# Performance work log

Measured on AMD Instinct MI355X. Metric: run time of the kernel, lower is better.

Reference implementation:

```python
import jax, jax.numpy as jnp
import numpy as np

B, T, DIM = 2, 4096, 2048
H, HKV = 16, 4
HD = DIM // H          # 128
NREP = H // HKV        # 4
R = 16                 # csa_compress_ratio
TOPK = 64              # min(csa_top_k, max_seq_len // R)
THETA = 10000.0


def setup_inputs() -> dict:
    key = jax.random.key(0)
    ks = jax.random.split(key, 9)
    s = 0.02
    return {
        "x":   jax.random.normal(ks[0], (B, T, DIM), jnp.float32),
        "wq":  jax.random.normal(ks[1], (DIM, H * HD),  jnp.float32) * s,
        "wk":  jax.random.normal(ks[2], (DIM, HKV * HD), jnp.float32) * s,
        "wv":  jax.random.normal(ks[3], (DIM, HKV * HD), jnp.float32) * s,
        "wo":  jax.random.normal(ks[4], (DIM, DIM), jnp.float32) * s,
        "wiq": jax.random.normal(ks[5], (DIM, HD), jnp.float32) * s,
        "wik": jax.random.normal(ks[6], (DIM, HD), jnp.float32) * s,
        "cwa": jax.random.normal(ks[7], (HD,), jnp.float32) * s,
        "cwb": jax.random.normal(ks[8], (HD,), jnp.float32) * s,
    }


def _rope(x, cos, sin):
    # x: [B, h, T, HD]; pairs (x[2i], x[2i+1]) rotated by angle[t, i]
    half = HD // 2
    xr = x.reshape(*x.shape[:-1], half, 2)
    a, b = xr[..., 0], xr[..., 1]          # [B, h, T, half]
    ra = a * cos - b * sin                 # cos/sin: [T, half] broadcast
    rb = a * sin + b * cos
    return jnp.stack([ra, rb], axis=-1).reshape(x.shape)


def reference(x, wq, wk, wv, wo, wiq, wik, cwa, cwb):
    Bx, Tx, C = x.shape
    half = HD // 2
    # RoPE tables (buffer in original, deterministic -> recomputed here)
    freqs = 1.0 / (THETA ** (jnp.arange(half, dtype=jnp.float32) / half))
    ang = jnp.arange(Tx, dtype=jnp.float32)[:, None] * freqs[None, :]  # [T, half]
    cos, sin = jnp.cos(ang), jnp.sin(ang)

    q = (x @ wq).reshape(Bx, Tx, H, HD).transpose(0, 2, 1, 3)    # [B,H,T,HD]
    k = (x @ wk).reshape(Bx, Tx, HKV, HD).transpose(0, 2, 1, 3)  # [B,HKV,T,HD]
    v = (x @ wv).reshape(Bx, Tx, HKV, HD).transpose(0, 2, 1, 3)
    q = _rope(q, cos, sin)
    k = _rope(k, cos, sin)

    # chunked softmax-weighted KV compression (vectorized over blocks)
    nb = Tx // R
    kb = k.reshape(Bx, HKV, nb, R, HD)
    vb = v.reshape(Bx, HKV, nb, R, HD)
    wa = jax.nn.softmax(kb @ cwa, axis=-1)   # [B,HKV,nb,R], softmax within block
    wb_ = jax.nn.softmax(kb @ cwb, axis=-1)
    w = 0.5 * (wa + wb_)
    ck = jnp.einsum('bhnr,bhnrd->bhnd', w, kb)  # [B,HKV,nb,HD]
    cv = jnp.einsum('bhnr,bhnrd->bhnd', w, vb)

    # indexer: scores[b,t] = mean_j( qi[b,t] . ki[b,j] ) = qi[b,t] . mean_j ki[b,j]
    qi = x @ wiq                         # [B,T,HD]
    ki_mean = (x @ wik).mean(axis=1)     # [B,HD]
    scores = jnp.einsum('btd,bd->bt', qi, ki_mean)  # [B,T]
    block_scores = scores[:, :nb]                   # [B,nb]

    if nb > TOPK:
        idx = jax.lax.top_k(block_scores, TOPK)[1]             # [B,TOPK]
        ck = jnp.take_along_axis(ck, idx[:, None, :, None], axis=2)  # [B,HKV,TOPK,HD]
        cv = jnp.take_along_axis(cv, idx[:, None, :, None], axis=2)

    # GQA repeat + sparse attention over selected compressed blocks (no mask)
    k_rep = jnp.repeat(ck, NREP, axis=1)   # [B,H,TOPK,HD]
    v_rep = jnp.repeat(cv, NREP, axis=1)
    att = jax.nn.softmax(
        jnp.einsum('bhtd,bhsd->bhts', q, k_rep) / jnp.sqrt(jnp.float32(HD)),
        axis=-1)                            # [B,H,T,TOPK]
    out = jnp.einsum('bhts,bhsd->bhtd', att, v_rep)
    out = out.transpose(0, 2, 1, 3).reshape(Bx, Tx, C)
    return out @ wo
```

## Files before the change

### kernel.cpp

```cpp
#include <hip/hip_runtime.h>
#include <math.h>
#include <stdint.h>

#define BB    2
#define TT    4096
#define CDIM  2048
#define NHQ   16
#define NKV   4
#define HD    128
#define HALF  64
#define NREP  4
#define RBLK  16
#define NB    256
#define TOPK  64

#define MROWS (BB * TT)
#define NQKV  (CDIM + 2 * NKV * HD)
#define XELE  ((size_t)MROWS * CDIM)

typedef __bf16 bf16;
typedef __bf16 bf16x4 __attribute__((ext_vector_type(4)));
typedef __bf16 bf16x8 __attribute__((ext_vector_type(8)));
typedef float f32x4 __attribute__((ext_vector_type(4)));

typedef __attribute__((address_space(1))) unsigned int gu32;
typedef __attribute__((address_space(3))) unsigned int lu32;

__device__ __forceinline__ void gload_lds16(const void* g, void* l) {
  void* gv = const_cast<void*>(g);
  __builtin_amdgcn_global_load_lds((gu32*)gv, (lu32*)l, 16, 0, 0);
}

__device__ __forceinline__ void mfma3_core(const bf16* __restrict__ Ah,
                                           const bf16* __restrict__ Al,
                                           const bf16* __restrict__ Bh,
                                           const bf16* __restrict__ Bl,
                                           int K, int bm, int bn,
                                           f32x4 acc[8][4]) {
  __shared__ bf16 sAh[256 * 32];
  __shared__ bf16 sAl[256 * 32];
  __shared__ bf16 sBh[128 * 32];
  __shared__ bf16 sBl[128 * 32];
  const int tid = threadIdx.x;
  const int wave = tid >> 6, lane = tid & 63;
  const int wr = wave >> 1, wc = wave & 1;
  const int fr = lane & 15, lg = lane >> 4;
  const int lr4 = lane >> 2;
  const int cgs = (lane & 3) ^ ((lane >> 3) & 3);
  const size_t stageoff = (size_t)lr4 * K + cgs * 8;

  const bf16* gAh = Ah + (size_t)bm * K + stageoff;
  const bf16* gAl = Al + (size_t)bm * K + stageoff;
  const bf16* gBh = Bh + (size_t)bn * K + stageoff;
  const bf16* gBl = Bl + (size_t)bn * K + stageoff;

  const int swf = (fr >> 1) & 3;
  const int aoffe = (wr * 128 + fr) * 32 + ((lg ^ swf) << 3);
  const int boffe = (wc * 64 + fr) * 32 + ((lg ^ swf) << 3);

  for (int k0 = 0; k0 < K; k0 += 32) {
    __syncthreads();
    if (wave == 0) {
#pragma unroll
      for (int u = 0; u < 12; ++u)
        gload_lds16(gAh + (size_t)(u * 16) * K + k0, sAh + u * 512);
    } else if (wave == 1) {
#pragma unroll
      for (int u = 12; u < 16; ++u)
        gload_lds16(gAh + (size_t)(u * 16) * K + k0, sAh + u * 512);
#pragma unroll
      for (int u = 0; u < 8; ++u)
        gload_lds16(gAl + (size_t)(u * 16) * K + k0, sAl + u * 512);
    } else if (wave == 2) {
#pragma unroll
      for (int u = 8; u < 16; ++u)
        gload_lds16(gAl + (size_t)(u * 16) * K + k0, sAl + u * 512);
#pragma unroll
      for (int u = 0; u < 4; ++u)
        gload_lds16(gBh + (size_t)(u * 16) * K + k0, sBh + u * 512);
    } else {
#pragma unroll
      for (int u = 4; u < 8; ++u)
        gload_lds16(gBh + (size_t)(u * 16) * K + k0, sBh + u * 512);
#pragma unroll
      for (int u = 0; u < 8; ++u)
        gload_lds16(gBl + (size_t)(u * 16) * K + k0, sBl + u * 512);
    }
    __syncthreads();
    bf16x8 fah[8], fal[8];
#pragma unroll
    for (int i = 0; i < 8; ++i) {
      fah[i] = *(const bf16x8*)&sAh[aoffe + i * 512];
      fal[i] = *(const bf16x8*)&sAl[aoffe + i * 512];
    }
#pragma unroll
    for (int j = 0; j < 4; ++j) {
      bf16x8 fbh = *(const bf16x8*)&sBh[boffe + j * 512];
      bf16x8 fbl = *(const bf16x8*)&sBl[boffe + j * 512];
#pragma unroll
      for (int i = 0; i < 8; ++i) {
        acc[i][j] = __builtin_amdgcn_mfma_f32_16x16x32_bf16(fah[i], fbh, acc[i][j], 0, 0, 0);
        acc[i][j] = __builtin_amdgcn_mfma_f32_16x16x32_bf16(fah[i], fbl, acc[i][j], 0, 0, 0);
        acc[i][j] = __builtin_amdgcn_mfma_f32_16x16x32_bf16(fal[i], fbh, acc[i][j], 0, 0, 0);
      }
    }
  }
}

__global__ __launch_bounds__(256, 2) void csa_gemm_qkv(const bf16* __restrict__ xh,
                                                       const bf16* __restrict__ xl,
                                                       const bf16* __restrict__ wth,
                                                       const bf16* __restrict__ wtl,
                                                       float* __restrict__ qb,
                                                       float* __restrict__ kb,
                                                       float* __restrict__ vb) {
  f32x4 acc[8][4] = {};
  const int bm = blockIdx.y << 8, bn = blockIdx.x << 7;
  mfma3_core(xh, xl, wth, wtl, CDIM, bm, bn, acc);
  const int wave = threadIdx.x >> 6, lane = threadIdx.x & 63;
  const int wr = wave >> 1, wc = wave & 1;
  const int fr = lane & 15, lg = lane >> 4;
  float* dst; int ncols, colofs;
  if (bn < CDIM)            { dst = qb; ncols = CDIM; colofs = bn; }
  else if (bn < CDIM + 512) { dst = kb; ncols = 512;  colofs = bn - CDIM; }
  else                      { dst = vb; ncols = 512;  colofs = bn - CDIM - 512; }
#pragma unroll
  for (int i = 0; i < 8; ++i)
#pragma unroll
    for (int j = 0; j < 4; ++j) {
      int row0 = bm + wr * 128 + i * 16 + (lg << 2);
      int col = colofs + wc * 64 + j * 16 + fr;
#pragma unroll
      for (int r = 0; r < 4; ++r)
        dst[(size_t)(row0 + r) * ncols + col] = acc[i][j][r];
    }
}

__global__ __launch_bounds__(256, 2) void csa_gemm_wo(const bf16* __restrict__ ah,
                                                      const bf16* __restrict__ al,
                                                      const bf16* __restrict__ wth,
                                                      const bf16* __restrict__ wtl,
                                                      float* __restrict__ C) {
  f32x4 acc[8][4] = {};
  const int bm = blockIdx.y << 8, bn = blockIdx.x << 7;
  mfma3_core(ah, al, wth, wtl, CDIM, bm, bn, acc);
  const int wave = threadIdx.x >> 6, lane = threadIdx.x & 63;
  const int wr = wave >> 1, wc = wave & 1;
  const int fr = lane & 15, lg = lane >> 4;
#pragma unroll
  for (int i = 0; i < 8; ++i)
#pragma unroll
    for (int j = 0; j < 4; ++j) {
      int row0 = bm + wr * 128 + i * 16 + (lg << 2);
      int col = bn + wc * 64 + j * 16 + fr;
#pragma unroll
      for (int r = 0; r < 4; ++r)
        C[(size_t)(row0 + r) * CDIM + col] = acc[i][j][r];
    }
}

__global__ void csa_xconv(const float4* __restrict__ x, bf16x4* __restrict__ xh,
                          bf16x4* __restrict__ xl) {
  int i = blockIdx.x * 256 + threadIdx.x;
  float4 v = x[i];
  bf16x4 h, l;
  h[0] = (bf16)v.x; l[0] = (bf16)(v.x - (float)h[0]);
  h[1] = (bf16)v.y; l[1] = (bf16)(v.y - (float)h[1]);
  h[2] = (bf16)v.z; l[2] = (bf16)(v.z - (float)h[2]);
  h[3] = (bf16)v.w; l[3] = (bf16)(v.w - (float)h[3]);
  xh[i] = h;
  xl[i] = l;
}

__global__ __launch_bounds__(256) void csa_wconv(const float* __restrict__ W, int N,
                                                 bf16* __restrict__ wth,
                                                 bf16* __restrict__ wtl, int rowofs) {
  __shared__ float tile[32][33];
  int k0 = blockIdx.y * 32, n0 = blockIdx.x * 32;
  int tx = threadIdx.x & 31, ty = threadIdx.x >> 5;
#pragma unroll
  for (int r = 0; r < 32; r += 8)
    tile[ty + r][tx] = W[(size_t)(k0 + ty + r) * N + n0 + tx];
  __syncthreads();
#pragma unroll
  for (int r = 0; r < 32; r += 8) {
    int n = ty + r;
    float x = tile[tx][n];
    bf16 h = (bf16)x;
    bf16 l = (bf16)(x - (float)h);
    size_t o = (size_t)(rowofs + n0 + n) * CDIM + k0 + tx;
    wth[o] = h;
    wtl[o] = l;
  }
}

__global__ void csa_rope_table(float* __restrict__ cost, float* __restrict__ sint) {
  int idx = blockIdx.x * blockDim.x + threadIdx.x;
  if (idx >= TT * HALF) return;
  int t = idx / HALF, i = idx % HALF;
  double freq = pow(10000.0, -(double)i / (double)HALF);
  double ang = (double)t * freq;
  cost[idx] = (float)cos(ang);
  sint[idx] = (float)sin(ang);
}

__global__ void csa_rope_apply(float* __restrict__ buf, const float* __restrict__ cost,
                               const float* __restrict__ sint, int nheads, int total) {
  int idx = blockIdx.x * blockDim.x + threadIdx.x;
  if (idx >= total) return;
  int i = idx % HALF;
  int h = (idx / HALF) % nheads;
  int t = (idx / (HALF * nheads)) % TT;
  int b = idx / (HALF * nheads * TT);
  float c = cost[t * HALF + i], s = sint[t * HALF + i];
  float* p = buf + ((((size_t)b * TT + t) * nheads + h) * HD) + 2 * i;
  float a = p[0], q = p[1];
  p[0] = a * c - q * s;
  p[1] = a * s + q * c;
}

__global__ void csa_xpart(const float* __restrict__ x, float* __restrict__ xpart) {
  int d = blockIdx.x * 256 + threadIdx.x;
  int ts = blockIdx.y;
  int b = blockIdx.z;
  float s = 0.f;
  int t0 = ts * (TT / 16);
  for (int t = t0; t < t0 + TT / 16; ++t) s += x[((size_t)b * TT + t) * CDIM + d];
  xpart[((size_t)b * 16 + ts) * CDIM + d] = s;
}

__global__ void csa_kimean(const float* __restrict__ xpart, const float* __restrict__ wik,
                           float* __restrict__ ki) {
  int b = blockIdx.x >> 7;
  int j = blockIdx.x & 127;
  int tid = threadIdx.x;
  float s = 0.f;
  for (int d = tid; d < CDIM; d += 256) {
    float xm = 0.f;
#pragma unroll
    for (int ts = 0; ts < 16; ++ts) xm += xpart[((size_t)b * 16 + ts) * CDIM + d];
    s += xm * wik[(size_t)d * HD + j];
  }
  __shared__ float red[256];
  red[tid] = s;
  __syncthreads();
  for (int off = 128; off > 0; off >>= 1) {
    if (tid < off) red[tid] += red[tid + off];
    __syncthreads();
  }
  if (tid == 0) ki[b * HD + j] = red[0] * (1.f / (float)TT);
}

__global__ void csa_u(const float* __restrict__ wiq, const float* __restrict__ ki,
                      float* __restrict__ u) {
  int idx = blockIdx.x * 256 + threadIdx.x;
  int b = idx / CDIM, d = idx % CDIM;
  float s = 0.f;
#pragma unroll 8
  for (int j = 0; j < HD; ++j) s += wiq[(size_t)d * HD + j] * ki[b * HD + j];
  u[idx] = s;
}

__global__ void csa_scores(const float* __restrict__ x, const float* __restrict__ u,
                           float* __restrict__ sc) {
  int b = blockIdx.x >> 8;
  int t = blockIdx.x & 255;
  int tid = threadIdx.x;
  float s = 0.f;
  for (int d = tid; d < CDIM; d += 256)
    s += x[((size_t)b * TT + t) * CDIM + d] * u[b * CDIM + d];
  __shared__ float red[256];
  red[tid] = s;
  __syncthreads();
  for (int off = 128; off > 0; off >>= 1) {
    if (tid < off) red[tid] += red[tid + off];
    __syncthreads();
  }
  if (tid == 0) sc[blockIdx.x] = red[0];
}

__global__ void csa_topk(const float* __restrict__ sc, int* __restrict__ topk) {
  __shared__ float val[NB];
  __shared__ float rv[256];
  __shared__ int ri[256];
  int b = blockIdx.x, tid = threadIdx.x;
  val[tid] = sc[b * NB + tid];
  __syncthreads();
  for (int it = 0; it < TOPK; ++it) {
    rv[tid] = val[tid];
    ri[tid] = tid;
    __syncthreads();
    for (int off = 128; off > 0; off >>= 1) {
      if (tid < off) {
        if (rv[tid + off] > rv[tid] ||
            (rv[tid + off] == rv[tid] && ri[tid + off] < ri[tid])) {
          rv[tid] = rv[tid + off];
          ri[tid] = ri[tid + off];
        }
      }
      __syncthreads();
    }
    if (tid == 0) {
      topk[b * TOPK + it] = ri[0];
      val[ri[0]] = -INFINITY;
    }
    __syncthreads();
  }
}

__global__ __launch_bounds__(64) void csa_compress(const float* __restrict__ kbuf,
                                                   const float* __restrict__ vbuf,
                                                   const int* __restrict__ topk,
                                                   const float* __restrict__ cwa,
                                                   const float* __restrict__ cwb,
                                                   bf16* __restrict__ ckh,
                                                   bf16* __restrict__ ckl,
                                                   bf16* __restrict__ cvth,
                                                   bf16* __restrict__ cvtl) {
  int blk = blockIdx.x;
  int b = blk / (NKV * TOPK);
  int h = (blk / TOPK) % NKV;
  int j = blk % TOPK;
  int n = topk[b * TOPK + j];
  int l = threadIdx.x;
  float ca0 = cwa[l], ca1 = cwa[l + 64];
  float cb0 = cwb[l], cb1 = cwb[l + 64];
  float kk[RBLK][2], vv[RBLK][2], ar[RBLK], br[RBLK];
#pragma unroll
  for (int r = 0; r < RBLK; ++r) {
    int t = n * RBLK + r;
    size_t base = (((size_t)b * TT + t) * NKV + h) * HD;
    kk[r][0] = kbuf[base + l];
    kk[r][1] = kbuf[base + l + 64];
    vv[r][0] = vbuf[base + l];
    vv[r][1] = vbuf[base + l + 64];
    float pa = kk[r][0] * ca0 + kk[r][1] * ca1;
    float pb = kk[r][0] * cb0 + kk[r][1] * cb1;
    for (int off = 32; off > 0; off >>= 1) {
      pa += __shfl_xor(pa, off);
      pb += __shfl_xor(pb, off);
    }
    ar[r] = pa;
    br[r] = pb;
  }
  float ma = -INFINITY, mb = -INFINITY;
#pragma unroll
  for (int r = 0; r < RBLK; ++r) { ma = fmaxf(ma, ar[r]); mb = fmaxf(mb, br[r]); }
  float ea[RBLK], eb[RBLK], sa = 0.f, sb = 0.f;
#pragma unroll
  for (int r = 0; r < RBLK; ++r) {
    ea[r] = expf(ar[r] - ma); sa += ea[r];
    eb[r] = expf(br[r] - mb); sb += eb[r];
  }
  float isa = 1.f / sa, isb = 1.f / sb;
  float o0 = 0.f, o1 = 0.f, p0 = 0.f, p1 = 0.f;
#pragma unroll
  for (int r = 0; r < RBLK; ++r) {
    float w = 0.5f * (ea[r] * isa + eb[r] * isb);
    o0 += w * kk[r][0]; o1 += w * kk[r][1];
    p0 += w * vv[r][0]; p1 += w * vv[r][1];
  }
  size_t ckbase = ((size_t)(b * NKV + h) * 64 + j) * 128;
  bf16 h0 = (bf16)o0; ckh[ckbase + l] = h0;      ckl[ckbase + l] = (bf16)(o0 - (float)h0);
  bf16 h1 = (bf16)o1; ckh[ckbase + l + 64] = h1; ckl[ckbase + l + 64] = (bf16)(o1 - (float)h1);
  size_t vtbase = (size_t)(b * NKV + h) * (128 * 64);
  bf16 g0 = (bf16)p0; cvth[vtbase + (size_t)l * 64 + j] = g0;
  cvtl[vtbase + (size_t)l * 64 + j] = (bf16)(p0 - (float)g0);
  bf16 g1 = (bf16)p1; cvth[vtbase + (size_t)(l + 64) * 64 + j] = g1;
  cvtl[vtbase + (size_t)(l + 64) * 64 + j] = (bf16)(p1 - (float)g1);
}

__global__ __launch_bounds__(256) void csa_attn_mfma(const float* __restrict__ qb,
                                                     const float* __restrict__ cost,
                                                     const float* __restrict__ sint,
                                                     const bf16* __restrict__ ckh_g,
                                                     const bf16* __restrict__ ckl_g,
                                                     const bf16* __restrict__ cvth_g,
                                                     const bf16* __restrict__ cvtl_g,
                                                     bf16* __restrict__ oh_g,
                                                     bf16* __restrict__ ol_g) {
  __shared__ __align__(16) bf16 sck[2][64 * 128];
  __shared__ __align__(16) bf16 sV[2][64 * 64];
  const int tid = threadIdx.x;
  const int wave = tid >> 6, lane = tid & 63;
  const int b = blockIdx.y >> 2, kvh = blockIdx.y & 3;
  const int row0 = blockIdx.x << 7;
  const int wrow = wave << 5;
  const int lr = lane & 15, lg = lane >> 4;
  const float scale = 0.08838834764831845f;

  const bf16* gkh = ckh_g + (size_t)(b * NKV + kvh) * (64 * 128);
  const bf16* gkl = ckl_g + (size_t)(b * NKV + kvh) * (64 * 128);
  const bf16* gvh = cvth_g + (size_t)(b * NKV + kvh) * (128 * 64);
  const bf16* gvl = cvtl_g + (size_t)(b * NKV + kvh) * (128 * 64);

  for (int idx = tid; idx < 1024; idx += 256) {
    int j = idx >> 4, c = idx & 15;
    int dst = (j * 16 + (c ^ (j & 15))) * 8;
    *(uint4*)&sck[0][dst] = *(const uint4*)(gkh + j * 128 + c * 8);
    *(uint4*)&sck[1][dst] = *(const uint4*)(gkl + j * 128 + c * 8);
  }
  for (int idx = tid; idx < 512; idx += 256) {
    int d = idx >> 3, c = idx & 7;
    int dst = (d * 8 + (c ^ (d & 7))) * 8;
    *(uint4*)&sV[0][dst] = *(const uint4*)(gvh + d * 64 + c * 8);
    *(uint4*)&sV[1][dst] = *(const uint4*)(gvl + d * 64 + c * 8);
  }

  bf16x8 qfh[2][4], qfl[2][4];
#pragma unroll
  for (int it = 0; it < 2; ++it)
#pragma unroll
    for (int ks = 0; ks < 4; ++ks) {
      int row = wrow + it * 16 + lr;
      int g = row0 + row;
      int t = g >> 2;
      int hh = kvh * NREP + (g & 3);
      int d0 = ks * 32 + (lg << 3);
      const float* qp = qb + (((size_t)b * TT + t) * NHQ + hh) * HD + d0;
      float4 a = *(const float4*)qp;
      float4 b4 = *(const float4*)(qp + 4);
      float4 cs = *(const float4*)&cost[t * HALF + (d0 >> 1)];
      float4 sn = *(const float4*)&sint[t * HALF + (d0 >> 1)];
      float f[8];
      f[0] = a.x * cs.x - a.y * sn.x;  f[1] = a.x * sn.x + a.y * cs.x;
      f[2] = a.z * cs.y - a.w * sn.y;  f[3] = a.z * sn.y + a.w * cs.y;
      f[4] = b4.x * cs.z - b4.y * sn.z; f[5] = b4.x * sn.z + b4.y * cs.z;
      f[6] = b4.z * cs.w - b4.w * sn.w; f[7] = b4.z * sn.w + b4.w * cs.w;
      bf16x8 h8, l8;
#pragma unroll
      for (int u = 0; u < 8; ++u) {
        h8[u] = (bf16)f[u];
        l8[u] = (bf16)(f[u] - (float)h8[u]);
      }
      qfh[it][ks] = h8;
      qfl[it][ks] = l8;
    }
  __syncthreads();

  f32x4 accS[2][4] = {};
#pragma unroll
  for (int ks = 0; ks < 4; ++ks) {
    bf16x8 kh[4], kl[4];
#pragma unroll
    for (int jt = 0; jt < 4; ++jt) {
      int row = jt * 16 + lr;
      int c = ks * 4 + lg;
      int off = (row * 16 + (c ^ (row & 15))) * 8;
      kh[jt] = *(const bf16x8*)&sck[0][off];
      kl[jt] = *(const bf16x8*)&sck[1][off];
    }
#pragma unroll
    for (int it = 0; it < 2; ++it)
#pragma unroll
      for (int jt = 0; jt < 4; ++jt) {
        accS[it][jt] = __builtin_amdgcn_mfma_f32_16x16x32_bf16(qfh[it][ks], kh[jt], accS[it][jt], 0, 0, 0);
        accS[it][jt] = __builtin_amdgcn_mfma_f32_16x16x32_bf16(qfh[it][ks], kl[jt], accS[it][jt], 0, 0, 0);
        accS[it][jt] = __builtin_amdgcn_mfma_f32_16x16x32_bf16(qfl[it][ks], kh[jt], accS[it][jt], 0, 0, 0);
      }
  }

#pragma unroll
  for (int it = 0; it < 2; ++it)
#pragma unroll
    for (int r = 0; r < 4; ++r) {
      float v0 = accS[it][0][r] * scale, v1 = accS[it][1][r] * scale;
      float v2 = accS[it][2][r] * scale, v3 = accS[it][3][r] * scale;
      float m = fmaxf(fmaxf(v0, v1), fmaxf(v2, v3));
      for (int off = 8; off > 0; off >>= 1) m = fmaxf(m, __shfl_xor(m, off));
      float e0 = expf(v0 - m), e1 = expf(v1 - m), e2 = expf(v2 - m), e3 = expf(v3 - m);
      float s = e0 + e1 + e2 + e3;
      for (int off = 8; off > 0; off >>= 1) s += __shfl_xor(s, off);
      float inv = 1.f / s;
      accS[it][0][r] = e0 * inv; accS[it][1][r] = e1 * inv;
      accS[it][2][r] = e2 * inv; accS[it][3][r] = e3 * inv;
    }

  __syncthreads();

#pragma unroll
  for (int it = 0; it < 2; ++it)
#pragma unroll
    for (int jt = 0; jt < 4; ++jt)
#pragma unroll
      for (int r = 0; r < 4; ++r) {
        int row = wrow + it * 16 + (lg << 2) + r;
        int k = jt * 16 + lr;
        float p = accS[it][jt][r];
        bf16 ph = (bf16)p;
        int c = k >> 3;
        int off = (row * 8 + (c ^ (row & 7))) * 8 + (k & 7);
        sck[0][off] = ph;
        sck[1][off] = (bf16)(p - (float)ph);
      }
  __syncthreads();

  for (int half = 0; half < 2; ++half) {
    if (half) {
      __syncthreads();
      for (int idx = tid; idx < 512; idx += 256) {
        int d = idx >> 3, c = idx & 7;
        int dst = (d * 8 + (c ^ (d & 7))) * 8;
        *(uint4*)&sV[0][dst] = *(const uint4*)(gvh + (64 + d) * 64 + c * 8);
        *(uint4*)&sV[1][dst] = *(const uint4*)(gvl + (64 + d) * 64 + c * 8);
      }
      __syncthreads();
    }
    f32x4 accO[2][4] = {};
#pragma unroll
    for (int ks = 0; ks < 2; ++ks) {
      bf16x8 pah[2], pal[2], vh[4], vl[4];
#pragma unroll
      for (int it = 0; it < 2; ++it) {
        int row = wrow + it * 16 + lr;
        int c = ks * 4 + lg;
        int off = (row * 8 + (c ^ (row & 7))) * 8;
        pah[it] = *(const bf16x8*)&sck[0][off];
        pal[it] = *(const bf16x8*)&sck[1][off];
      }
#pragma unroll
      for (int jt = 0; jt < 4; ++jt) {
        int d = jt * 16 + lr;
        int c = ks * 4 + lg;
        int off = (d * 8 + (c ^ (d & 7))) * 8;
        vh[jt] = *(const bf16x8*)&sV[0][off];
        vl[jt] = *(const bf16x8*)&sV[1][off];
      }
#pragma unroll
      for (int it = 0; it < 2; ++it)
#pragma unroll
        for (int jt = 0; jt < 4; ++jt) {
          accO[it][jt] = __builtin_amdgcn_mfma_f32_16x16x32_bf16(pah[it], vh[jt], accO[it][jt], 0, 0, 0);
          accO[it][jt] = __builtin_amdgcn_mfma_f32_16x16x32_bf16(pah[it], vl[jt], accO[it][jt], 0, 0, 0);
          accO[it][jt] = __builtin_amdgcn_mfma_f32_16x16x32_bf16(pal[it], vh[jt], accO[it][jt], 0, 0, 0);
        }
    }
#pragma unroll
    for (int it = 0; it < 2; ++it)
#pragma unroll
      for (int jt = 0; jt < 4; ++jt)
#pragma unroll
        for (int r = 0; r < 4; ++r) {
          int row = wrow + it * 16 + (lg << 2) + r;
          int g = row0 + row;
          int t = g >> 2;
          int hh = kvh * NREP + (g & 3);
          size_t ob = (((size_t)b * TT + t) * NHQ + hh) * HD + half * 64 + jt * 16 + lr;
          float o = accO[it][jt][r];
          bf16 oh = (bf16)o;
          oh_g[ob] = oh;
          ol_g[ob] = (bf16)(o - (float)oh);
        }
  }
}

extern "C" void kernel_launch(void* const* d_in, const int* in_sizes, int n_in,
                              void* d_out, int out_size, void* d_ws, size_t ws_size,
                              hipStream_t stream) {
  const float* x   = (const float*)d_in[0];
  const float* wq  = (const float*)d_in[1];
  const float* wk  = (const float*)d_in[2];
  const float* wv  = (const float*)d_in[3];
  const float* wo  = (const float*)d_in[4];
  const float* wiq = (const float*)d_in[5];
  const float* wik = (const float*)d_in[6];
  const float* cwa = (const float*)d_in[7];
  const float* cwb = (const float*)d_in[8];
  float* out = (float*)d_out;

  float* qb = out;

  float* ws = (float*)d_ws;
  float* kb   = ws;
  float* vb   = kb + (size_t)MROWS * 512;
  bf16*  xh   = (bf16*)(vb + (size_t)MROWS * 512);
  bf16*  xl   = xh + XELE;
  bf16*  wqh  = xl + XELE;
  bf16*  wql  = wqh + (size_t)NQKV * CDIM;
  float* cost = (float*)(wql + (size_t)NQKV * CDIM);
  float* sint = cost + (size_t)TT * HALF;
  float* xpart = sint + (size_t)TT * HALF;
  float* ki   = xpart + (size_t)BB * 16 * CDIM;
  float* u    = ki + BB * HD;
  float* sc   = u + BB * CDIM;
  bf16*  ckh  = (bf16*)(sc + BB * NB);
  bf16*  ckl  = ckh + (size_t)BB * NKV * 64 * 128;
  bf16*  cvth = ckl + (size_t)BB * NKV * 64 * 128;
  bf16*  cvtl = cvth + (size_t)BB * NKV * 128 * 64;
  int* topk   = (int*)(cvtl + (size_t)BB * NKV * 128 * 64);
  bf16* oh  = xh;
  bf16* ol_ = xl;
  bf16* woh = wqh;
  bf16* wol = wql;

  csa_xconv<<<(XELE / 4) / 256, 256, 0, stream>>>((const float4*)x, (bf16x4*)xh, (bf16x4*)xl);
  csa_wconv<<<dim3(CDIM / 32, CDIM / 32), 256, 0, stream>>>(wq, CDIM, wqh, wql, 0);
  csa_wconv<<<dim3(512 / 32, CDIM / 32), 256, 0, stream>>>(wk, 512, wqh, wql, CDIM);
  csa_wconv<<<dim3(512 / 32, CDIM / 32), 256, 0, stream>>>(wv, 512, wqh, wql, CDIM + 512);

  csa_gemm_qkv<<<dim3(NQKV / 128, MROWS / 256), 256, 0, stream>>>(xh, xl, wqh, wql, qb, kb, vb);

  csa_wconv<<<dim3(CDIM / 32, CDIM / 32), 256, 0, stream>>>(wo, CDIM, woh, wol, 0);

  csa_rope_table<<<(TT * HALF + 255) / 256, 256, 0, stream>>>(cost, sint);
  csa_rope_apply<<<(BB * TT * NKV * HALF + 255) / 256, 256, 0, stream>>>(kb, cost, sint, NKV, BB * TT * NKV * HALF);

  csa_xpart<<<dim3(CDIM / 256, 16, BB), 256, 0, stream>>>(x, xpart);
  csa_kimean<<<BB * HD, 256, 0, stream>>>(xpart, wik, ki);
  csa_u<<<(BB * CDIM) / 256, 256, 0, stream>>>(wiq, ki, u);
  csa_scores<<<BB * NB, 256, 0, stream>>>(x, u, sc);
  csa_topk<<<BB, 256, 0, stream>>>(sc, topk);

  csa_compress<<<BB * NKV * TOPK, 64, 0, stream>>>(kb, vb, topk, cwa, cwb, ckh, ckl, cvth, cvtl);

  csa_attn_mfma<<<dim3((TT * NREP) / 128, BB * NKV), 256, 0, stream>>>(qb, cost, sint, ckh, ckl, cvth, cvtl, oh, ol_);

  csa_gemm_wo<<<dim3(CDIM / 128, MROWS / 256), 256, 0, stream>>>(oh, ol_, woh, wol, out);
}
```

Before: 792.1 us.

## Double-buffer GEMM LDS tiles with 8-wave blocks and async prefetch

```diff
diff --git a/kernel.cpp b/kernel.cpp
--- a/kernel.cpp
+++ b/kernel.cpp
@@ -31,92 +31,104 @@
   __builtin_amdgcn_global_load_lds((gu32*)gv, (lu32*)l, 16, 0, 0);
 }
 
-__device__ __forceinline__ void mfma3_core(const bf16* __restrict__ Ah,
-                                           const bf16* __restrict__ Al,
-                                           const bf16* __restrict__ Bh,
-                                           const bf16* __restrict__ Bl,
-                                           int K, int bm, int bn,
-                                           f32x4 acc[8][4]) {
-  __shared__ bf16 sAh[256 * 32];
-  __shared__ bf16 sAl[256 * 32];
-  __shared__ bf16 sBh[128 * 32];
-  __shared__ bf16 sBl[128 * 32];
+
+#define LDS_BUF 24576
+#define OFF_AL  8192
+#define OFF_BH  16384
+#define OFF_BL  20480
+
+__device__ __forceinline__ void mfma3_step(const bf16* __restrict__ sb, int arow,
+                                           int brow, int chunk, f32x4 acc[4][4]) {
+  bf16x8 fah[4], fal[4], fbh[4], fbl[4];
+#pragma unroll
+  for (int i = 0; i < 4; ++i) {
+    fah[i] = *(const bf16x8*)&sb[(arow + i * 16) * 32 + chunk];
+    fal[i] = *(const bf16x8*)&sb[OFF_AL + (arow + i * 16) * 32 + chunk];
+  }
+#pragma unroll
+  for (int j = 0; j < 4; ++j) {
+    fbh[j] = *(const bf16x8*)&sb[OFF_BH + (brow + j * 16) * 32 + chunk];
+    fbl[j] = *(const bf16x8*)&sb[OFF_BL + (brow + j * 16) * 32 + chunk];
+  }
+  __builtin_amdgcn_s_setprio(1);
+#pragma unroll
+  for (int j = 0; j < 4; ++j)
+#pragma unroll
+    for (int i = 0; i < 4; ++i) {
+      acc[i][j] = __builtin_amdgcn_mfma_f32_16x16x32_bf16(fah[i], fbh[j], acc[i][j], 0, 0, 0);
+      acc[i][j] = __builtin_amdgcn_mfma_f32_16x16x32_bf16(fah[i], fbl[j], acc[i][j], 0, 0, 0);
+      acc[i][j] = __builtin_amdgcn_mfma_f32_16x16x32_bf16(fal[i], fbh[j], acc[i][j], 0, 0, 0);
+    }
+  __builtin_amdgcn_s_setprio(0);
+}
+
+__device__ __forceinline__ void mfma3_core8(const bf16* __restrict__ Ah,
+                                            const bf16* __restrict__ Al,
+                                            const bf16* __restrict__ Bh,
+                                            const bf16* __restrict__ Bl,
+                                            int bm, int bn,
+                                            f32x4 acc[4][4]) {
+  __shared__ __align__(16) bf16 smem[2 * LDS_BUF];
   const int tid = threadIdx.x;
   const int wave = tid >> 6, lane = tid & 63;
+  const int lr4 = lane >> 2;
+  const int cgs = (lane & 3) ^ ((lane >> 3) & 3);
+  const size_t stageoff = (size_t)lr4 * CDIM + cgs * 8;
+
+  const bf16* gp[6];
+  int loff[6];
+#pragma unroll
+  for (int u = 0; u < 6; ++u) {
+    int c = wave * 6 + u;
+    const bf16* base;
+    int lbase;
+    if (c < 16)      { base = Ah + (size_t)(bm + c * 16) * CDIM;        lbase = c * 512; }
+    else if (c < 32) { base = Al + (size_t)(bm + (c - 16) * 16) * CDIM; lbase = OFF_AL + (c - 16) * 512; }
+    else if (c < 40) { base = Bh + (size_t)(bn + (c - 32) * 16) * CDIM; lbase = OFF_BH + (c - 32) * 512; }
+    else             { base = Bl + (size_t)(bn + (c - 40) * 16) * CDIM; lbase = OFF_BL + (c - 40) * 512; }
+    gp[u] = base + stageoff;
+    loff[u] = lbase;
+  }
+
   const int wr = wave >> 1, wc = wave & 1;
   const int fr = lane & 15, lg = lane >> 4;
-  const int lr4 = lane >> 2;
-  const int cgs = (lane & 3) ^ ((lane >> 3) & 3);
-  const size_t stageoff = (size_t)lr4 * K + cgs * 8;
-
-  const bf16* gAh = Ah + (size_t)bm * K + stageoff;
-  const bf16* gAl = Al + (size_t)bm * K + stageoff;
-  const bf16* gBh = Bh + (size_t)bn * K + stageoff;
-  const bf16* gBl = Bl + (size_t)bn * K + stageoff;
-
-  const int swf = (fr >> 1) & 3;
-  const int aoffe = (wr * 128 + fr) * 32 + ((lg ^ swf) << 3);
-  const int boffe = (wc * 64 + fr) * 32 + ((lg ^ swf) << 3);
-
-  for (int k0 = 0; k0 < K; k0 += 32) {
-    __syncthreads();
-    if (wave == 0) {
-#pragma unroll
-      for (int u = 0; u < 12; ++u)
-        gload_lds16(gAh + (size_t)(u * 16) * K + k0, sAh + u * 512);
-    } else if (wave == 1) {
-#pragma unroll
-      for (int u = 12; u < 16; ++u)
-        gload_lds16(gAh + (size_t)(u * 16) * K + k0, sAh + u * 512);
-#pragma unroll
-      for (int u = 0; u < 8; ++u)
-        gload_lds16(gAl + (size_t)(u * 16) * K + k0, sAl + u * 512);
-    } else if (wave == 2) {
-#pragma unroll
-      for (int u = 8; u < 16; ++u)
-        gload_lds16(gAl + (size_t)(u * 16) * K + k0, sAl + u * 512);
-#pragma unroll
-      for (int u = 0; u < 4; ++u)
-        gload_lds16(gBh + (size_t)(u * 16) * K + k0, sBh + u * 512);
-    } else {
-#pragma unroll
-      for (int u = 4; u < 8; ++u)
-        gload_lds16(gBh + (size_t)(u * 16) * K + k0, sBh + u * 512);
-#pragma unroll
-      for (int u = 0; u < 8; ++u)
-        gload_lds16(gBl + (size_t)(u * 16) * K + k0, sBl + u * 512);
-    }
-    __syncthreads();
-    bf16x8 fah[8], fal[8];
-#pragma unroll
-    for (int i = 0; i < 8; ++i) {
-      fah[i] = *(const bf16x8*)&sAh[aoffe + i * 512];
-      fal[i] = *(const bf16x8*)&sAl[aoffe + i * 512];
-    }
-#pragma unroll
-    for (int j = 0; j < 4; ++j) {
-      bf16x8 fbh = *(const bf16x8*)&sBh[boffe + j * 512];
-      bf16x8 fbl = *(const bf16x8*)&sBl[boffe + j * 512];
-#pragma unroll
-      for (int i = 0; i < 8; ++i) {
-        acc[i][j] = __builtin_amdgcn_mfma_f32_16x16x32_bf16(fah[i], fbh, acc[i][j], 0, 0, 0);
-        acc[i][j] = __builtin_amdgcn_mfma_f32_16x16x32_bf16(fah[i], fbl, acc[i][j], 0, 0, 0);
-        acc[i][j] = __builtin_amdgcn_mfma_f32_16x16x32_bf16(fal[i], fbh, acc[i][j], 0, 0, 0);
-      }
-    }
-  }
-}
-
-__global__ __launch_bounds__(256, 2) void csa_gemm_qkv(const bf16* __restrict__ xh,
+  const int chunk = (lg ^ ((fr >> 1) & 3)) << 3;
+  const int arow = wr * 64 + fr;
+  const int brow = wc * 64 + fr;
+
+#pragma unroll
+  for (int u = 0; u < 6; ++u) gload_lds16(gp[u], &smem[loff[u]]);
+
+  for (int t = 0; t < 63; ++t) {
+    const int nbase = ((t + 1) & 1) * LDS_BUF;
+    const int kk = (t + 1) * 32;
+#pragma unroll
+    for (int u = 0; u < 6; ++u) gload_lds16(gp[u] + kk, &smem[nbase + loff[u]]);
+    asm volatile("s_waitcnt vmcnt(6)" ::: "memory");
+    __builtin_amdgcn_s_barrier();
+    asm volatile("" ::: "memory");
+
+    mfma3_step(&smem[(t & 1) * LDS_BUF], arow, brow, chunk, acc);
+
+    asm volatile("" ::: "memory");
+    __builtin_amdgcn_s_barrier();
+  }
+  asm volatile("s_waitcnt vmcnt(0)" ::: "memory");
+  __builtin_amdgcn_s_barrier();
+  asm volatile("" ::: "memory");
+  mfma3_step(&smem[LDS_BUF], arow, brow, chunk, acc);
+}
+
+__global__ __launch_bounds__(512, 2) void csa_gemm_qkv(const bf16* __restrict__ xh,
                                                        const bf16* __restrict__ xl,
                                                        const bf16* __restrict__ wth,
                                                        const bf16* __restrict__ wtl,
                                                        float* __restrict__ qb,
                                                        float* __restrict__ kb,
                                                        float* __restrict__ vb) {
-  f32x4 acc[8][4] = {};
+  f32x4 acc[4][4] = {};
   const int bm = blockIdx.y << 8, bn = blockIdx.x << 7;
-  mfma3_core(xh, xl, wth, wtl, CDIM, bm, bn, acc);
+  mfma3_core8(xh, xl, wth, wtl, bm, bn, acc);
   const int wave = threadIdx.x >> 6, lane = threadIdx.x & 63;
   const int wr = wave >> 1, wc = wave & 1;
   const int fr = lane & 15, lg = lane >> 4;
@@ -125,10 +137,10 @@
   else if (bn < CDIM + 512) { dst = kb; ncols = 512;  colofs = bn - CDIM; }
   else                      { dst = vb; ncols = 512;  colofs = bn - CDIM - 512; }
 #pragma unroll
-  for (int i = 0; i < 8; ++i)
+  for (int i = 0; i < 4; ++i)
 #pragma unroll
     for (int j = 0; j < 4; ++j) {
-      int row0 = bm + wr * 128 + i * 16 + (lg << 2);
+      int row0 = bm + wr * 64 + i * 16 + (lg << 2);
       int col = colofs + wc * 64 + j * 16 + fr;
 #pragma unroll
       for (int r = 0; r < 4; ++r)
@@ -136,22 +148,22 @@
     }
 }
 
-__global__ __launch_bounds__(256, 2) void csa_gemm_wo(const bf16* __restrict__ ah,
+__global__ __launch_bounds__(512, 2) void csa_gemm_wo(const bf16* __restrict__ ah,
                                                       const bf16* __restrict__ al,
                                                       const bf16* __restrict__ wth,
                                                       const bf16* __restrict__ wtl,
                                                       float* __restrict__ C) {
-  f32x4 acc[8][4] = {};
+  f32x4 acc[4][4] = {};
   const int bm = blockIdx.y << 8, bn = blockIdx.x << 7;
-  mfma3_core(ah, al, wth, wtl, CDIM, bm, bn, acc);
+  mfma3_core8(ah, al, wth, wtl, bm, bn, acc);
   const int wave = threadIdx.x >> 6, lane = threadIdx.x & 63;
   const int wr = wave >> 1, wc = wave & 1;
   const int fr = lane & 15, lg = lane >> 4;
 #pragma unroll
-  for (int i = 0; i < 8; ++i)
+  for (int i = 0; i < 4; ++i)
 #pragma unroll
     for (int j = 0; j < 4; ++j) {
-      int row0 = bm + wr * 128 + i * 16 + (lg << 2);
+      int row0 = bm + wr * 64 + i * 16 + (lg << 2);
       int col = bn + wc * 64 + j * 16 + fr;
 #pragma unroll
       for (int r = 0; r < 4; ++r)
@@ -598,7 +610,7 @@
   csa_wconv<<<dim3(512 / 32, CDIM / 32), 256, 0, stream>>>(wk, 512, wqh, wql, CDIM);
   csa_wconv<<<dim3(512 / 32, CDIM / 32), 256, 0, stream>>>(wv, 512, wqh, wql, CDIM + 512);
 
-  csa_gemm_qkv<<<dim3(NQKV / 128, MROWS / 256), 256, 0, stream>>>(xh, xl, wqh, wql, qb, kb, vb);
+  csa_gemm_qkv<<<dim3(NQKV / 128, MROWS / 256), 512, 0, stream>>>(xh, xl, wqh, wql, qb, kb, vb);
 
   csa_wconv<<<dim3(CDIM / 32, CDIM / 32), 256, 0, stream>>>(wo, CDIM, woh, wol, 0);
 
@@ -615,5 +627,5 @@
 
   csa_attn_mfma<<<dim3((TT * NREP) / 128, BB * NKV), 256, 0, stream>>>(qb, cost, sint, ckh, ckl, cvth, cvtl, oh, ol_);
 
-  csa_gemm_wo<<<dim3(CDIM / 128, MROWS / 256), 256, 0, stream>>>(oh, ol_, woh, wol, out);
-}
+  csa_gemm_wo<<<dim3(CDIM / 128, MROWS / 256), 512, 0, stream>>>(oh, ol_, woh, wol, out);
+}
```

Measured after the change: 804.9 us. No clear change (+1.6%).
